# Kernel optimization log

Hardware: AMD Instinct MI355X
Metric: run time of the kernel (lower is better)

## Reference

```python
import jax, jax.numpy as jnp
import numpy as np

NUM_HEAD = 8
HIDDEN = 128
INPUT_DIM = 256
N1 = 1024
N2 = 1024
BATCH = 16


def setup_inputs() -> dict:
    key = jax.random.key(0)
    ks = jax.random.split(key, 10)
    HD = HIDDEN * NUM_HEAD  # 1024
    return {
        "x1": jax.random.normal(ks[0], (BATCH, N1, INPUT_DIM), jnp.float32),
        "x2": jax.random.normal(ks[1], (BATCH, N2, INPUT_DIM), jnp.float32),
        "B": jax.random.normal(ks[2], (N1, N2), jnp.float32),
        "wq_w": jax.random.normal(ks[3], (HD, INPUT_DIM), jnp.float32) * 0.02,
        "wq_b": jnp.zeros((HD,), jnp.float32),
        "wk_w": jax.random.normal(ks[4], (HD, INPUT_DIM), jnp.float32) * 0.02,
        "wk_b": jnp.zeros((HD,), jnp.float32),
        "wv_w": jax.random.normal(ks[5], (HD, INPUT_DIM), jnp.float32) * 0.02,
        "wv_b": jnp.zeros((HD,), jnp.float32),
        "proj_w": jax.random.normal(ks[6], (HIDDEN, HD), jnp.float32) * 0.02,
        "proj_b": jnp.zeros((HIDDEN,), jnp.float32),
    }


def reference(x1, x2, B, wq_w, wq_b, wk_w, wk_b, wv_w, wv_b, proj_w, proj_b):
    b, n1, _ = x1.shape
    n2 = x2.shape[1]
    sdk = jnp.sqrt(jnp.asarray(HIDDEN, x1.dtype))
    # Linear layers (torch convention: y = x @ W.T + b)
    q = x1 @ wq_w.T + wq_b                      # [b, n1, H*D]
    k = x2 @ wk_w.T + wk_b                      # [b, n2, H*D]
    v = x2 @ wv_w.T + wv_b                      # [b, n2, H*D]
    q = q.reshape(b, n1, NUM_HEAD, HIDDEN)
    k = k.reshape(b, n2, NUM_HEAD, HIDDEN)
    v = v.reshape(b, n2, NUM_HEAD, HIDDEN)
    # scores: [b, h, n1, n2]
    scores = jnp.einsum("bnhd,bmhd->bhnm", q, k) / sdk + B[None, None, :, :]
    attn = jax.nn.softmax(scores, axis=-1)
    out = jnp.einsum("bhnm,bmhd->bnhd", attn, v).reshape(b, n1, NUM_HEAD * HIDDEN)
    return out @ proj_w.T + proj_b              # [b, n1, HIDDEN]
```

## Files before the change

### kernel.cpp

```cpp
#include <hip/hip_runtime.h>
#include <hip/hip_fp16.h>

typedef _Float16 f16;
typedef __attribute__((ext_vector_type(4))) _Float16 f16x4;
typedef __attribute__((ext_vector_type(8))) _Float16 f16x8;
typedef __attribute__((ext_vector_type(4))) float f32x4;

#define MFMA_F16(a,b,c) __builtin_amdgcn_mfma_f32_16x16x32_f16((a),(b),(c),0,0,0)

__device__ __forceinline__ void gl_lds16(const f16* g, f16* l) {
  __builtin_amdgcn_global_load_lds(
      (const __attribute__((address_space(1))) unsigned int*)g,
      (__attribute__((address_space(3))) unsigned int*)l, 16, 0, 0);
}


__global__ __launch_bounds__(256) void conv_pack(
    const float* __restrict__ x1, const float* __restrict__ x2,
    const float* __restrict__ wq, const float* __restrict__ wk,
    const float* __restrict__ wv,
    f16* __restrict__ x1p, f16* __restrict__ x2p, f16* __restrict__ wp) {
  __shared__ f16 S[128][264];
  const int id = blockIdx.x, tid = threadIdx.x;
  const float* src;
  f16* dst;
  if (id < 128) {
    src = x1 + (size_t)id * 32768; dst = x1p + (size_t)id * 32768;
  } else if (id < 256) {
    src = x2 + (size_t)(id - 128) * 32768; dst = x2p + (size_t)(id - 128) * 32768;
  } else {
    const int wsel = (id - 256) >> 3, wt = (id - 256) & 7;
    const float* wsrc = (wsel == 0) ? wq : (wsel == 1) ? wk : wv;
    src = wsrc + (size_t)wt * 32768;
    dst = wp + (size_t)wsel * 262144 + (size_t)wt * 32768;
  }
#pragma unroll 8
  for (int i = 0; i < 32; i++) {
    int f = i * 256 + tid;
    int row = f >> 6, c4 = f & 63;
    float4 v = *(const float4*)(src + (size_t)row * 256 + c4 * 4);
    f16x4 hh; hh[0] = (f16)v.x; hh[1] = (f16)v.y; hh[2] = (f16)v.z; hh[3] = (f16)v.w;
    *(f16x4*)&S[row][c4 * 4] = hh;
  }
  __syncthreads();
#pragma unroll 8
  for (int i = 0; i < 16; i++) {
    int u = i * 256 + tid;
    int chunk = u >> 6, l2 = u & 63;
    int q = l2 >> 4, c = l2 & 15;
    int row = (chunk >> 3) * 16 + c, k = (chunk & 7) * 32 + q * 8;
    f16x8 v = *(const f16x8*)&S[row][k];
    *(f16x8*)(dst + (size_t)u * 8) = v;
  }
}

__global__ __launch_bounds__(512) __attribute__((amdgpu_waves_per_eu(4, 4)))
void gemm_qkv(const f16* __restrict__ x1p, const f16* __restrict__ x2p,
              const f16* __restrict__ wp,
              const float* __restrict__ wqb, const float* __restrict__ wkb,
              const float* __restrict__ wvb,
              f16* __restrict__ Qp, f16* __restrict__ Kp, f16* __restrict__ Vp,
              float qscale) {
  __shared__ f16 Wl[2][8192];
  __shared__ f16 Xl[2][8192];
  const int z = blockIdx.z;
  const f16* Xp = (z == 0) ? x1p : x2p;
  const float* bias = (z == 0) ? wqb : (z == 1) ? wkb : wvb;
  f16* outp = (z == 0) ? Qp : (z == 1) ? Kp : Vp;
  const float sc = (z == 0) ? qscale : 1.0f;

  const int tid = threadIdx.x, lane = tid & 63, wid = tid >> 6;
  const int col = lane & 15, quad = lane >> 4;
  const int xt = blockIdx.x, h = blockIdx.y;
  const int wr = wid >> 2, xc = wid & 3;
  const f16* Xb = Xp + (size_t)xt * 32768;
  const f16* Wb = wp + (size_t)z * 262144 + (size_t)h * 32768;

#define QISSUE(T, bufi)                                                   \
  {                                                                       \
    _Pragma("unroll") for (int j = 0; j < 2; j++) {                       \
      int lc = wid * 2 + j;                                               \
      int rt = lc >> 1, ksl = lc & 1;                                     \
      gl_lds16(Wb + (size_t)((rt * 8 + (T) * 2 + ksl) << 9) + lane * 8,   \
               &Wl[bufi][lc * 512]);                                      \
      gl_lds16(Xb + (size_t)((rt * 8 + (T) * 2 + ksl) << 9) + lane * 8,   \
               &Xl[bufi][lc * 512]);                                      \
    }                                                                     \
  }

  QISSUE(0, 0);
  QISSUE(1, 1);

  f32x4 acc[4][2];
#pragma unroll
  for (int i = 0; i < 4; i++)
#pragma unroll
    for (int j = 0; j < 2; j++) acc[i][j] = (f32x4){0.f, 0.f, 0.f, 0.f};

  __syncthreads();

  for (int t = 0; t < 4; ++t) {
    const int buf = t & 1;
    const f16* Ra = (z == 2) ? Xl[buf] : Wl[buf];
    const f16* Cb = (z == 2) ? Wl[buf] : Xl[buf];
#pragma unroll
    for (int ksl = 0; ksl < 2; ksl++) {
      f16x8 af[4], bf[2];
#pragma unroll
      for (int i = 0; i < 4; i++)
        af[i] = *(const f16x8*)&Ra[((wr * 4 + i) * 2 + ksl) * 512 + lane * 8];
#pragma unroll
      for (int j = 0; j < 2; j++)
        bf[j] = *(const f16x8*)&Cb[((xc * 2 + j) * 2 + ksl) * 512 + lane * 8];
#pragma unroll
      for (int i = 0; i < 4; i++)
#pragma unroll
        for (int j = 0; j < 2; j++) acc[i][j] = MFMA_F16(af[i], bf[j], acc[i][j]);
    }
    __syncthreads();
    if (t + 2 < 4) QISSUE(t + 2, buf);
  }

  if (z < 2) {
#pragma unroll
    for (int i = 0; i < 4; i++) {
      const int k0h = wr * 64 + i * 16 + quad * 4;
      float4 bq = *(const float4*)(bias + h * 128 + k0h);
      const int ks2 = k0h >> 5, q2 = (k0h >> 3) & 3, lo = k0h & 7;
#pragma unroll
      for (int j = 0; j < 2; j++) {
        const int bn2 = xt * 128 + xc * 32 + j * 16 + col;
        const int b = bn2 >> 10, n2 = bn2 & 1023;
        const int T = n2 >> 6, jt = (n2 >> 4) & 3, c2 = n2 & 15;
        f16x4 pk;
#pragma unroll
        for (int r = 0; r < 4; r++)
          pk[r] = (f16)((acc[i][j][r] + ((const float*)&bq)[r]) * sc);
        *(f16x4*)(outp + (size_t)(b * 8 + h) * 131072 + T * 8192 +
                  (jt * 4 + ks2) * 512 + (q2 * 16 + c2) * 8 + lo) = pk;
      }
    }
  } else {
#pragma unroll
    for (int j = 0; j < 2; j++) {
      const int d = xc * 32 + j * 16 + col;
      const float bv = bias[h * 128 + d];
      const int ct = d >> 4, cc = d & 15;
#pragma unroll
      for (int i = 0; i < 4; i++) {
        const int bn2 = xt * 128 + wr * 64 + i * 16 + quad * 4;
        const int b = bn2 >> 10, n2 = bn2 & 1023;
        const int T = n2 >> 6, kv6 = n2 & 63;
        const int ks2 = kv6 >> 5, qv = (kv6 >> 3) & 3, jj = kv6 & 7;
        f16x4 pk;
#pragma unroll
        for (int r = 0; r < 4; r++) pk[r] = (f16)(acc[i][j][r] + bv);
        *(f16x4*)(outp + (size_t)(b * 8 + h) * 131072 + T * 8192 +
                  (ct * 2 + ks2) * 512 + (qv * 16 + cc) * 8 + jj) = pk;
      }
    }
  }
}

__global__ __launch_bounds__(256) void gemm_proj(const f16* __restrict__ A,
                                                 const float* __restrict__ W,
                                                 const float* __restrict__ bias,
                                                 float* __restrict__ out) {
  constexpr int LD = 72;
  __shared__ f16 As[64][LD];
  __shared__ f16 Bs[64][LD];
  const int tid = threadIdx.x, lane = tid & 63, wid = tid >> 6;
  const int col = lane & 15, quad = lane >> 4;
  const int wm = (wid >> 1) * 32, wn = (wid & 1) * 32;
  const int m0 = blockIdx.x * 64, n0 = blockIdx.y * 64;

  f32x4 acc[2][2];
#pragma unroll
  for (int i = 0; i < 2; i++)
#pragma unroll
    for (int j = 0; j < 2; j++) acc[i][j] = (f32x4){0.f, 0.f, 0.f, 0.f};

  for (int kt = 0; kt < 16; ++kt) {
    const int k0 = kt * 64;
#pragma unroll
    for (int i = 0; i < 2; i++) {
      int f = i * 256 + tid;
      int r = f >> 3, ch = f & 7;
      *(f16x8*)&As[r][ch * 8] = *(const f16x8*)(A + (size_t)(m0 + r) * 1024 + k0 + ch * 8);
    }
#pragma unroll
    for (int i = 0; i < 4; i++) {
      int f = i * 256 + tid;
      int r = f >> 4, c4 = f & 15;
      float4 v = *(const float4*)(W + (size_t)(n0 + r) * 1024 + k0 + c4 * 4);
      f16x4 hh; hh[0] = (f16)v.x; hh[1] = (f16)v.y; hh[2] = (f16)v.z; hh[3] = (f16)v.w;
      *(f16x4*)&Bs[r][c4 * 4] = hh;
    }
    __syncthreads();
#pragma unroll
    for (int ks = 0; ks < 2; ks++) {
      f16x8 af[2], bf[2];
#pragma unroll
      for (int i = 0; i < 2; i++) af[i] = *(const f16x8*)&As[wm + i * 16 + col][ks * 32 + quad * 8];
#pragma unroll
      for (int j = 0; j < 2; j++) bf[j] = *(const f16x8*)&Bs[wn + j * 16 + col][ks * 32 + quad * 8];
#pragma unroll
      for (int i = 0; i < 2; i++)
#pragma unroll
        for (int j = 0; j < 2; j++) acc[i][j] = MFMA_F16(af[i], bf[j], acc[i][j]);
    }
    __syncthreads();
  }
#pragma unroll
  for (int j = 0; j < 2; j++) {
    const int c = n0 + wn + j * 16 + col;
    const float bv = bias[c];
#pragma unroll
    for (int i = 0; i < 2; i++) {
      const int r0 = m0 + wm + i * 16 + quad * 4;
#pragma unroll
      for (int r = 0; r < 4; r++)
        out[(size_t)(r0 + r) * 128 + c] = acc[i][j][r] + bv;
    }
  }
}

__global__ __launch_bounds__(256, 2)
void attn_fused(const f16* __restrict__ Qp, const f16* __restrict__ Kp,
                const f16* __restrict__ Vp, const float* __restrict__ Bm,
                f16* __restrict__ O) {
  __shared__ f16 Ksl[2][8192];
  __shared__ f16 Vtl[2][8192];
  __shared__ f16 Ps[8192];
  const int tid = threadIdx.x, lane = tid & 63, wid = tid >> 6;
  const int col = lane & 15, quad = lane >> 4;
  const int id = blockIdx.x;
  const int mt = (id >> 3) & 7;
  const int bh = ((id >> 6) << 3) | (id & 7);
  const int b = bh >> 3, h = bh & 7;
  const int m0 = mt * 128;
  const int wm = wid * 32;

  const f16* Qb = Qp + (size_t)bh * 131072;
  const f16* Kb = Kp + (size_t)bh * 131072;
  const f16* Vb = Vp + (size_t)bh * 131072;

#define AISSUE(T, bufi)                                                       \
  {                                                                           \
    if (wid < 2) {                                                            \
      _Pragma("unroll") for (int j = 0; j < 8; j++)                           \
          gl_lds16(Kb + (size_t)(T) * 8192 + (wid * 8 + j) * 512 + lane * 8,  \
                   &Ksl[bufi][(wid * 8 + j) * 512]);                          \
    } else {                                                                  \
      _Pragma("unroll") for (int j = 0; j < 8; j++)                           \
          gl_lds16(Vb + (size_t)(T) * 8192 + ((wid - 2) * 8 + j) * 512 + lane * 8, \
                   &Vtl[bufi][((wid - 2) * 8 + j) * 512]);                    \
    }                                                                         \
  }

  AISSUE(0, 0);
  AISSUE(1, 1);

  f16x8 qf[2][4];
#pragma unroll
  for (int qc = 0; qc < 2; qc++) {
    const int m = m0 + wm + qc * 16;
    const int T = m >> 6, jt2 = (m >> 4) & 3;
#pragma unroll
    for (int ks = 0; ks < 4; ks++)
      qf[qc][ks] = *(const f16x8*)(Qb + T * 8192 + (jt2 * 4 + ks) * 512 + lane * 8);
  }

  f32x4 oacc[2][8];
  float l[2] = {0.f, 0.f};
#pragma unroll
  for (int qc = 0; qc < 2; qc++)
#pragma unroll
    for (int ct = 0; ct < 8; ct++) oacc[qc][ct] = (f32x4){0.f, 0.f, 0.f, 0.f};

  __syncthreads();

  for (int t = 0; t < 16; ++t) {
    const int buf = t & 1;
    const int n0 = t * 64;

    float4 breg[2][4];
#pragma unroll
    for (int qc = 0; qc < 2; qc++) {
      const float* Brow = Bm + (size_t)(m0 + wm + qc * 16 + col) * 1024 + n0;
#pragma unroll
      for (int jt = 0; jt < 4; jt++)
        breg[qc][jt] = *(const float4*)(Brow + jt * 16 + quad * 4);
    }

    f32x4 s[2][4];
#pragma unroll
    for (int qc = 0; qc < 2; qc++)
#pragma unroll
      for (int jt = 0; jt < 4; jt++) s[qc][jt] = (f32x4){0.f, 0.f, 0.f, 0.f};
#pragma unroll
    for (int ks = 0; ks < 4; ks++) {
      f16x8 kf[4];
#pragma unroll
      for (int jt = 0; jt < 4; jt++)
        kf[jt] = *(const f16x8*)&Ksl[buf][(jt * 4 + ks) * 512 + lane * 8];
#pragma unroll
      for (int jt = 0; jt < 4; jt++)
#pragma unroll
        for (int qc = 0; qc < 2; qc++)
          s[qc][jt] = MFMA_F16(kf[jt], qf[qc][ks], s[qc][jt]);
    }

#pragma unroll
    for (int qc = 0; qc < 2; qc++) {
      const int m = wm + qc * 16 + col;
#pragma unroll
      for (int jt = 0; jt < 4; jt++) {
        const float* bv = (const float*)&breg[qc][jt];
        float p0 = __expf(s[qc][jt][0] + bv[0]);
        float p1 = __expf(s[qc][jt][1] + bv[1]);
        float p2 = __expf(s[qc][jt][2] + bv[2]);
        float p3 = __expf(s[qc][jt][3] + bv[3]);
        l[qc] += (p0 + p1) + (p2 + p3);
        f16x4 pk; pk[0] = (f16)p0; pk[1] = (f16)p1; pk[2] = (f16)p2; pk[3] = (f16)p3;
        const int g = (jt * 2 + (quad >> 1)) ^ (col & 7);
        *(f16x4*)&Ps[m * 64 + g * 8 + (quad & 1) * 4] = pk;
      }
    }

#pragma unroll
    for (int ks = 0; ks < 2; ks++) {
      f16x8 pf[2];
#pragma unroll
      for (int qc = 0; qc < 2; qc++) {
        const int m = wm + qc * 16 + col;
        const int g = (ks * 4 + quad) ^ (col & 7);
        pf[qc] = *(const f16x8*)&Ps[m * 64 + g * 8];
      }
#pragma unroll
      for (int ct = 0; ct < 8; ct++) {
        f16x8 vf = *(const f16x8*)&Vtl[buf][(ct * 2 + ks) * 512 + lane * 8];
#pragma unroll
        for (int qc = 0; qc < 2; qc++)
          oacc[qc][ct] = MFMA_F16(pf[qc], vf, oacc[qc][ct]);
      }
    }

    __syncthreads();
    if (t + 2 < 16) AISSUE(t + 2, buf);
  }

#pragma unroll
  for (int qc = 0; qc < 2; qc++) {
    float lw = l[qc];
    lw += __shfl_xor(lw, 16);
    lw += __shfl_xor(lw, 32);
    f16* Ob = O + ((size_t)(b * 1024 + m0 + wm + qc * 16)) * 1024 + h * 128;
#pragma unroll
    for (int r = 0; r < 4; r++) {
      const float lv = __shfl(lw, (lane & 48) | (quad * 4 + r));
      const float inv = 1.0f / lv;
#pragma unroll
      for (int ct = 0; ct < 8; ct++)
        Ob[(size_t)(quad * 4 + r) * 1024 + ct * 16 + col] = (f16)(oacc[qc][ct][r] * inv);
    }
  }
}

extern "C" void kernel_launch(void* const* d_in, const int* in_sizes, int n_in,
                              void* d_out, int out_size, void* d_ws, size_t ws_size,
                              hipStream_t stream) {
  (void)in_sizes; (void)n_in; (void)out_size; (void)ws_size;
  const float* x1  = (const float*)d_in[0];
  const float* x2  = (const float*)d_in[1];
  const float* Bm  = (const float*)d_in[2];
  const float* wq  = (const float*)d_in[3];
  const float* wqb = (const float*)d_in[4];
  const float* wk  = (const float*)d_in[5];
  const float* wkb = (const float*)d_in[6];
  const float* wv  = (const float*)d_in[7];
  const float* wvb = (const float*)d_in[8];
  const float* pw  = (const float*)d_in[9];
  const float* pb  = (const float*)d_in[10];
  float* out = (float*)d_out;

  const size_t MiB = 1024 * 1024;
  f16* Qp  = (f16*)d_ws;
  f16* Kp  = (f16*)((char*)d_ws + 32 * MiB);
  f16* Vp  = (f16*)((char*)d_ws + 64 * MiB);
  f16* Ow  = (f16*)((char*)d_ws + 96 * MiB);
  f16* x1p = (f16*)((char*)d_ws + 96 * MiB);
  f16* x2p = (f16*)((char*)d_ws + 104 * MiB);
  f16* wp  = (f16*)((char*)d_ws + 112 * MiB);

  const float scale = 0.0883883476483184f;
  conv_pack<<<dim3(280), dim3(256), 0, stream>>>(x1, x2, wq, wk, wv, x1p, x2p, wp);
  gemm_qkv<<<dim3(128, 8, 3), dim3(512), 0, stream>>>(x1p, x2p, wp, wqb, wkb, wvb,
                                                      Qp, Kp, Vp, scale);
  attn_fused<<<dim3(1024), dim3(256), 0, stream>>>(Qp, Kp, Vp, Bm, Ow);
  gemm_proj<<<dim3(256, 2), dim3(256), 0, stream>>>(Ow, pw, pb, out);
}
```

Baseline: 277.4 us.

## Prepack bias matrix into MFMA fragment order and raise wave priority around MFMAs

Adds a pack_bias kernel that rewrites the 1024x1024 bias into per-tile, per-wave fragment order, so the attention loop reads it with fully coalesced float4 loads instead of strided row reads. The packed path is enabled only when the workspace is at least 132 MiB; otherwise the original load path is kept. It also brackets both MFMA phases with s_setprio to favour matrix issue over other waves. The cost is an extra small kernel launch and 4 MiB of extra workspace traffic.

```diff
diff --git a/kernel.cpp b/kernel.cpp
--- a/kernel.cpp
+++ b/kernel.cpp
@@ -54,6 +54,31 @@
   }
 }
 
+__global__ __launch_bounds__(256) void pack_bias(
+    const float* __restrict__ Bm, float* __restrict__ Bp) {
+  __shared__ float S[128][68];
+  const int id = blockIdx.x, tid = threadIdx.x;
+  const int mt = id >> 4, t = id & 15;
+  const int m0 = mt * 128, n0 = t * 64;
+#pragma unroll
+  for (int i = 0; i < 8; i++) {
+    int f = i * 256 + tid;
+    int r = f >> 4, c4 = f & 15;
+    float4 v = *(const float4*)(Bm + (size_t)(m0 + r) * 1024 + n0 + c4 * 4);
+    *(float4*)&S[r][c4 * 4] = v;
+  }
+  __syncthreads();
+  float4* out = (float4*)Bp + (size_t)id * 2048;
+#pragma unroll
+  for (int i = 0; i < 8; i++) {
+    int u = i * 256 + tid;
+    int lane = u & 63, jt = (u >> 6) & 3, qcw = u >> 8;
+    int col = lane & 15, quad = lane >> 4;
+    float4 v = *(const float4*)&S[qcw * 16 + col][jt * 16 + quad * 4];
+    out[u] = v;
+  }
+}
+
 __global__ __launch_bounds__(512) __attribute__((amdgpu_waves_per_eu(4, 4)))
 void gemm_qkv(const f16* __restrict__ x1p, const f16* __restrict__ x2p,
               const f16* __restrict__ wp,
@@ -228,6 +253,7 @@
 __global__ __launch_bounds__(256, 2)
 void attn_fused(const f16* __restrict__ Qp, const f16* __restrict__ Kp,
                 const f16* __restrict__ Vp, const float* __restrict__ Bm,
+                const float* __restrict__ Bp, const int use_packed,
                 f16* __restrict__ O) {
   __shared__ f16 Ksl[2][8192];
   __shared__ f16 Vtl[2][8192];
@@ -244,6 +270,7 @@
   const f16* Qb = Qp + (size_t)bh * 131072;
   const f16* Kb = Kp + (size_t)bh * 131072;
   const f16* Vb = Vp + (size_t)bh * 131072;
+  const float4* Bw = (const float4*)Bp + (size_t)mt * 16 * 2048 + (size_t)(wid * 2) * 256 + lane;
 
 #define AISSUE(T, bufi)                                                       \
   {                                                                           \
@@ -285,12 +312,21 @@
     const int n0 = t * 64;
 
     float4 breg[2][4];
-#pragma unroll
-    for (int qc = 0; qc < 2; qc++) {
-      const float* Brow = Bm + (size_t)(m0 + wm + qc * 16 + col) * 1024 + n0;
-#pragma unroll
-      for (int jt = 0; jt < 4; jt++)
-        breg[qc][jt] = *(const float4*)(Brow + jt * 16 + quad * 4);
+    if (use_packed) {
+      const float4* Bt = Bw + (size_t)t * 2048;
+#pragma unroll
+      for (int qc = 0; qc < 2; qc++)
+#pragma unroll
+        for (int jt = 0; jt < 4; jt++)
+          breg[qc][jt] = Bt[qc * 256 + jt * 64];
+    } else {
+#pragma unroll
+      for (int qc = 0; qc < 2; qc++) {
+        const float* Brow = Bm + (size_t)(m0 + wm + qc * 16 + col) * 1024 + n0;
+#pragma unroll
+        for (int jt = 0; jt < 4; jt++)
+          breg[qc][jt] = *(const float4*)(Brow + jt * 16 + quad * 4);
+      }
     }
 
     f32x4 s[2][4];
@@ -298,6 +334,7 @@
     for (int qc = 0; qc < 2; qc++)
 #pragma unroll
       for (int jt = 0; jt < 4; jt++) s[qc][jt] = (f32x4){0.f, 0.f, 0.f, 0.f};
+    __builtin_amdgcn_s_setprio(1);
 #pragma unroll
     for (int ks = 0; ks < 4; ks++) {
       f16x8 kf[4];
@@ -310,6 +347,7 @@
         for (int qc = 0; qc < 2; qc++)
           s[qc][jt] = MFMA_F16(kf[jt], qf[qc][ks], s[qc][jt]);
     }
+    __builtin_amdgcn_s_setprio(0);
 
 #pragma unroll
     for (int qc = 0; qc < 2; qc++) {
@@ -328,6 +366,7 @@
       }
     }
 
+    __builtin_amdgcn_s_setprio(1);
 #pragma unroll
     for (int ks = 0; ks < 2; ks++) {
       f16x8 pf[2];
@@ -345,6 +384,7 @@
           oacc[qc][ct] = MFMA_F16(pf[qc], vf, oacc[qc][ct]);
       }
     }
+    __builtin_amdgcn_s_setprio(0);
 
     __syncthreads();
     if (t + 2 < 16) AISSUE(t + 2, buf);
@@ -370,7 +410,7 @@
 extern "C" void kernel_launch(void* const* d_in, const int* in_sizes, int n_in,
                               void* d_out, int out_size, void* d_ws, size_t ws_size,
                               hipStream_t stream) {
-  (void)in_sizes; (void)n_in; (void)out_size; (void)ws_size;
+  (void)in_sizes; (void)n_in; (void)out_size;
   const float* x1  = (const float*)d_in[0];
   const float* x2  = (const float*)d_in[1];
   const float* Bm  = (const float*)d_in[2];
@@ -393,10 +433,15 @@
   f16* x2p = (f16*)((char*)d_ws + 104 * MiB);
   f16* wp  = (f16*)((char*)d_ws + 112 * MiB);
 
+  const int use_packed = (ws_size >= 132 * MiB) ? 1 : 0;
+  float* Bpk = use_packed ? (float*)((char*)d_ws + 128 * MiB) : (float*)Bm;
+
   const float scale = 0.0883883476483184f;
   conv_pack<<<dim3(280), dim3(256), 0, stream>>>(x1, x2, wq, wk, wv, x1p, x2p, wp);
+  if (use_packed)
+    pack_bias<<<dim3(128), dim3(256), 0, stream>>>(Bm, Bpk);
   gemm_qkv<<<dim3(128, 8, 3), dim3(512), 0, stream>>>(x1p, x2p, wp, wqb, wkb, wvb,
                                                       Qp, Kp, Vp, scale);
-  attn_fused<<<dim3(1024), dim3(256), 0, stream>>>(Qp, Kp, Vp, Bm, Ow);
+  attn_fused<<<dim3(1024), dim3(256), 0, stream>>>(Qp, Kp, Vp, Bm, Bpk, use_packed, Ow);
   gemm_proj<<<dim3(256, 2), dim3(256), 0, stream>>>(Ow, pw, pb, out);
 }
```

Result: slower. 316.0 us (+13.9%).

## Stage K/V tiles through registers instead of direct global-to-LDS loads

Applied to the files above, without the earlier changes.

Replaces the global_load_lds asynchronous copies of K and V tiles with register staging. Each wave loads the tile for step t+2 into registers and writes the step t+1 tile into the alternate LDS buffer at the top of the iteration. All four waves now share the copy work, and the barrier waits only on lgkmcnt instead of a full syncthreads. This adds register pressure and explicit LDS write instructions, but could hide global latency across a full iteration.

```diff
diff --git a/kernel.cpp b/kernel.cpp
--- a/kernel.cpp
+++ b/kernel.cpp
@@ -245,21 +245,34 @@
   const f16* Kb = Kp + (size_t)bh * 131072;
   const f16* Vb = Vp + (size_t)bh * 131072;
 
-#define AISSUE(T, bufi)                                                       \
+  f16x8 stK[4], stV[4];
+
+#define ALOAD(T)                                                              \
   {                                                                           \
-    if (wid < 2) {                                                            \
-      _Pragma("unroll") for (int j = 0; j < 8; j++)                           \
-          gl_lds16(Kb + (size_t)(T) * 8192 + (wid * 8 + j) * 512 + lane * 8,  \
-                   &Ksl[bufi][(wid * 8 + j) * 512]);                          \
-    } else {                                                                  \
-      _Pragma("unroll") for (int j = 0; j < 8; j++)                           \
-          gl_lds16(Vb + (size_t)(T) * 8192 + ((wid - 2) * 8 + j) * 512 + lane * 8, \
-                   &Vtl[bufi][((wid - 2) * 8 + j) * 512]);                    \
+    _Pragma("unroll") for (int j = 0; j < 4; j++) {                           \
+      stK[j] = *(const f16x8*)(Kb + (size_t)(T) * 8192 + (wid * 4 + j) * 512 + lane * 8); \
+      stV[j] = *(const f16x8*)(Vb + (size_t)(T) * 8192 + (wid * 4 + j) * 512 + lane * 8); \
     }                                                                         \
   }
 
-  AISSUE(0, 0);
-  AISSUE(1, 1);
+#define AWRITE(bufi)                                                          \
+  {                                                                           \
+    _Pragma("unroll") for (int j = 0; j < 4; j++) {                           \
+      *(f16x8*)&Ksl[bufi][(wid * 4 + j) * 512 + lane * 8] = stK[j];           \
+      *(f16x8*)&Vtl[bufi][(wid * 4 + j) * 512 + lane * 8] = stV[j];           \
+    }                                                                         \
+  }
+
+#define ABARRIER()                                                            \
+  {                                                                           \
+    asm volatile("s_waitcnt lgkmcnt(0)" ::: "memory");                        \
+    __builtin_amdgcn_s_barrier();                                             \
+    __builtin_amdgcn_sched_barrier(0);                                        \
+  }
+
+  ALOAD(0);
+  AWRITE(0);
+  ALOAD(1);
 
   f16x8 qf[2][4];
 #pragma unroll
@@ -278,12 +291,14 @@
 #pragma unroll
     for (int ct = 0; ct < 8; ct++) oacc[qc][ct] = (f32x4){0.f, 0.f, 0.f, 0.f};
 
-  __syncthreads();
+  ABARRIER();
 
   for (int t = 0; t < 16; ++t) {
     const int buf = t & 1;
     const int n0 = t * 64;
 
+    if (t + 1 < 16) AWRITE(buf ^ 1);
+
     float4 breg[2][4];
 #pragma unroll
     for (int qc = 0; qc < 2; qc++) {
@@ -292,6 +307,8 @@
       for (int jt = 0; jt < 4; jt++)
         breg[qc][jt] = *(const float4*)(Brow + jt * 16 + quad * 4);
     }
+
+    if (t + 2 < 16) ALOAD(t + 2);
 
     f32x4 s[2][4];
 #pragma unroll
@@ -346,8 +363,7 @@
       }
     }
 
-    __syncthreads();
-    if (t + 2 < 16) AISSUE(t + 2, buf);
+    ABARRIER();
   }
 
 #pragma unroll
```

After: 276.6 us. About the same (-0.3%).

## Precompute exp(B) as fp16 in fragment layout and multiply inside attention

Applied to the files above, without the earlier changes.

Adds a pack_eb kernel that computes exp(B) once, converts it to fp16 and stores it in the per-lane MFMA fragment order, using the output buffer as scratch. The attention kernel now loads half-size fp16 bias tiles with contiguous vector loads and multiplies exp(s) by the precomputed factor instead of adding B before exp. This cuts bias read bandwidth and exp work repeated across the 128 batch-heads. In exchange, exp(B) in fp16 can overflow or lose precision for large B, and the layout assumes the fixed 1024x1024 size.

```diff
diff --git a/kernel.cpp b/kernel.cpp
--- a/kernel.cpp
+++ b/kernel.cpp
@@ -54,6 +54,43 @@
   }
 }
 
+__global__ __launch_bounds__(256) void pack_eb(
+    const float* __restrict__ Bm, f16* __restrict__ Ebp) {
+  __shared__ float S[128][68];
+  const int id = blockIdx.x, tid = threadIdx.x;
+  const int mt = id >> 4, t = id & 15;
+  const int m0 = mt * 128, n0 = t * 64;
+#pragma unroll
+  for (int i = 0; i < 8; i++) {
+    int f = i * 256 + tid;
+    int r = f >> 4, c4 = f & 15;
+    float4 v = *(const float4*)(Bm + (size_t)(m0 + r) * 1024 + n0 + c4 * 4);
+    *(float4*)&S[r][c4 * 4] = v;
+  }
+  __syncthreads();
+#pragma unroll
+  for (int i = 0; i < 2; i++) {
+    int s = i * 256 + tid;
+    int qcw = s >> 6, lane = s & 63;
+    int col = lane & 15, quad = lane >> 4;
+    int row = qcw * 16 + col;
+    f16x8 h0, h1;
+#pragma unroll
+    for (int j = 0; j < 8; j++) {
+      int jt = j >> 2, r = j & 3;
+      h0[j] = (f16)__expf(S[row][jt * 16 + quad * 4 + r]);
+    }
+#pragma unroll
+    for (int j = 0; j < 8; j++) {
+      int jt = 2 + (j >> 2), r = j & 3;
+      h1[j] = (f16)__expf(S[row][jt * 16 + quad * 4 + r]);
+    }
+    f16* out = Ebp + (((size_t)id * 8 + qcw) * 64 + lane) * 16;
+    *(f16x8*)out = h0;
+    *(f16x8*)(out + 8) = h1;
+  }
+}
+
 __global__ __launch_bounds__(512) __attribute__((amdgpu_waves_per_eu(4, 4)))
 void gemm_qkv(const f16* __restrict__ x1p, const f16* __restrict__ x2p,
               const f16* __restrict__ wp,
@@ -227,7 +264,7 @@
 
 __global__ __launch_bounds__(256, 2)
 void attn_fused(const f16* __restrict__ Qp, const f16* __restrict__ Kp,
-                const f16* __restrict__ Vp, const float* __restrict__ Bm,
+                const f16* __restrict__ Vp, const f16* __restrict__ Ebp,
                 f16* __restrict__ O) {
   __shared__ f16 Ksl[2][8192];
   __shared__ f16 Vtl[2][8192];
@@ -244,6 +281,7 @@
   const f16* Qb = Qp + (size_t)bh * 131072;
   const f16* Kb = Kp + (size_t)bh * 131072;
   const f16* Vb = Vp + (size_t)bh * 131072;
+  const f16* Ebw = Ebp + (((size_t)mt * 16 * 8 + wid * 2) * 64 + lane) * 16;
 
 #define AISSUE(T, bufi)                                                       \
   {                                                                           \
@@ -282,15 +320,14 @@
 
   for (int t = 0; t < 16; ++t) {
     const int buf = t & 1;
-    const int n0 = t * 64;
-
-    float4 breg[2][4];
-#pragma unroll
-    for (int qc = 0; qc < 2; qc++) {
-      const float* Brow = Bm + (size_t)(m0 + wm + qc * 16 + col) * 1024 + n0;
-#pragma unroll
-      for (int jt = 0; jt < 4; jt++)
-        breg[qc][jt] = *(const float4*)(Brow + jt * 16 + quad * 4);
+
+    f16x8 ebA[2], ebB[2];
+    {
+      const f16* Et = Ebw + (size_t)t * (8 * 64 * 16);
+      ebA[0] = *(const f16x8*)(Et);
+      ebB[0] = *(const f16x8*)(Et + 8);
+      ebA[1] = *(const f16x8*)(Et + 1024);
+      ebB[1] = *(const f16x8*)(Et + 1032);
     }
 
     f32x4 s[2][4];
@@ -316,11 +353,18 @@
       const int m = wm + qc * 16 + col;
 #pragma unroll
       for (int jt = 0; jt < 4; jt++) {
-        const float* bv = (const float*)&breg[qc][jt];
-        float p0 = __expf(s[qc][jt][0] + bv[0]);
-        float p1 = __expf(s[qc][jt][1] + bv[1]);
-        float p2 = __expf(s[qc][jt][2] + bv[2]);
-        float p3 = __expf(s[qc][jt][3] + bv[3]);
+        float p0, p1, p2, p3;
+        if (jt < 2) {
+          p0 = __expf(s[qc][jt][0]) * (float)ebA[qc][(jt & 1) * 4 + 0];
+          p1 = __expf(s[qc][jt][1]) * (float)ebA[qc][(jt & 1) * 4 + 1];
+          p2 = __expf(s[qc][jt][2]) * (float)ebA[qc][(jt & 1) * 4 + 2];
+          p3 = __expf(s[qc][jt][3]) * (float)ebA[qc][(jt & 1) * 4 + 3];
+        } else {
+          p0 = __expf(s[qc][jt][0]) * (float)ebB[qc][(jt & 1) * 4 + 0];
+          p1 = __expf(s[qc][jt][1]) * (float)ebB[qc][(jt & 1) * 4 + 1];
+          p2 = __expf(s[qc][jt][2]) * (float)ebB[qc][(jt & 1) * 4 + 2];
+          p3 = __expf(s[qc][jt][3]) * (float)ebB[qc][(jt & 1) * 4 + 3];
+        }
         l[qc] += (p0 + p1) + (p2 + p3);
         f16x4 pk; pk[0] = (f16)p0; pk[1] = (f16)p1; pk[2] = (f16)p2; pk[3] = (f16)p3;
         const int g = (jt * 2 + (quad >> 1)) ^ (col & 7);
@@ -392,11 +436,13 @@
   f16* x1p = (f16*)((char*)d_ws + 96 * MiB);
   f16* x2p = (f16*)((char*)d_ws + 104 * MiB);
   f16* wp  = (f16*)((char*)d_ws + 112 * MiB);
+  f16* Ebp = (f16*)d_out;
 
   const float scale = 0.0883883476483184f;
   conv_pack<<<dim3(280), dim3(256), 0, stream>>>(x1, x2, wq, wk, wv, x1p, x2p, wp);
+  pack_eb<<<dim3(128), dim3(256), 0, stream>>>(Bm, Ebp);
   gemm_qkv<<<dim3(128, 8, 3), dim3(512), 0, stream>>>(x1p, x2p, wp, wqb, wkb, wvb,
                                                       Qp, Kp, Vp, scale);
-  attn_fused<<<dim3(1024), dim3(256), 0, stream>>>(Qp, Kp, Vp, Bm, Ow);
+  attn_fused<<<dim3(1024), dim3(256), 0, stream>>>(Qp, Kp, Vp, Ebp, Ow);
   gemm_proj<<<dim3(256, 2), dim3(256), 0, stream>>>(Ow, pw, pb, out);
 }
```

After: 266.0 us. -4.1%, faster.
